# Kernel tuning notes

Measured on AMD Instinct MI355X. Metric: run time of the kernel, lower is better.

Reference implementation:

```python
import jax, jax.numpy as jnp
import numpy as np

H = 4096  # input_size == hidden_size


def setup_inputs() -> dict:
    key = jax.random.key(0)
    ks = jax.random.split(key, 11)
    s = 1.0 / np.sqrt(2 * H)  # nn.Linear default init scale
    return {
        "h_tmin1": jax.random.normal(ks[0], (H,), jnp.float32),
        "c_tmin1": jax.random.normal(ks[1], (H,), jnp.float32),
        "x_t": jax.random.normal(ks[2], (H,), jnp.float32),
        "W_f": jax.random.uniform(ks[3], (H, 2 * H), jnp.float32, -s, s),
        "b_f": jax.random.uniform(ks[4], (H,), jnp.float32, -s, s),
        "W_i": jax.random.uniform(ks[5], (H, 2 * H), jnp.float32, -s, s),
        "b_i": jax.random.uniform(ks[6], (H,), jnp.float32, -s, s),
        "W_C": jax.random.uniform(ks[7], (H, 2 * H), jnp.float32, -s, s),
        "b_C": jax.random.uniform(ks[8], (H,), jnp.float32, -s, s),
        "W_o": jax.random.uniform(ks[9], (H, 2 * H), jnp.float32, -s, s),
        "b_o": jax.random.uniform(ks[10], (H,), jnp.float32, -s, s),
    }


def reference(h_tmin1, c_tmin1, x_t, W_f, b_f, W_i, b_i, W_C, b_C, W_o, b_o):
    # z_hx = cat([h, x]) used for f, i, o gates.
    z_hx = jnp.concatenate([h_tmin1, x_t])          # [2H]
    # Faithful quirk: original C_t calls Ctilde_t(h_tmin1, c_tmin1),
    # so the candidate gate sees cat([h, c]) instead of cat([h, x]).
    z_hc = jnp.concatenate([h_tmin1, c_tmin1])      # [2H]

    f = jax.nn.sigmoid(W_f @ z_hx + b_f)            # forget gate  [H]
    i = jax.nn.sigmoid(W_i @ z_hx + b_i)            # input gate   [H]
    Ctilde = jnp.tanh(W_C @ z_hc + b_C)             # candidate    [H]
    C = f * c_tmin1 + i * Ctilde                    # new cell     [H]
    o = jax.nn.sigmoid(W_o @ z_hx + b_o)            # output gate  [H]
    h = o * jnp.tanh(C)                             # new hidden   [H]
    # output() returns (hidden, cell); it recomputes C_t redundantly in the
    # original, which is mathematically identical to reusing C here.
    return (h, C)
```

## Files before the change

kernel.cpp:

```cpp
#include <hip/hip_runtime.h>
#include <math.h>

constexpr int H  = 4096;
constexpr int H2 = 8192;

__global__ __launch_bounds__(256, 4)
void lstm_step_kernel(const float* __restrict__ h_prev,
                      const float* __restrict__ c_prev,
                      const float* __restrict__ x_t,
                      const float* __restrict__ W_f, const float* __restrict__ b_f,
                      const float* __restrict__ W_i, const float* __restrict__ b_i,
                      const float* __restrict__ W_C, const float* __restrict__ b_C,
                      const float* __restrict__ W_o, const float* __restrict__ b_o,
                      float* __restrict__ out)
{
    const int gtid = blockIdx.x * blockDim.x + threadIdx.x;
    const int row  = gtid >> 6;
    const int lane = threadIdx.x & 63;
    if (row >= H) return;

    const float4* wf = (const float4*)(W_f + (size_t)row * H2);
    const float4* wi = (const float4*)(W_i + (size_t)row * H2);
    const float4* wc = (const float4*)(W_C + (size_t)row * H2);
    const float4* wo = (const float4*)(W_o + (size_t)row * H2);
    const float4* hv = (const float4*)h_prev;
    const float4* xv = (const float4*)x_t;
    const float4* cv = (const float4*)c_prev;

    float4 af = make_float4(0.f, 0.f, 0.f, 0.f);
    float4 ai = make_float4(0.f, 0.f, 0.f, 0.f);
    float4 ac = make_float4(0.f, 0.f, 0.f, 0.f);
    float4 ao = make_float4(0.f, 0.f, 0.f, 0.f);

    #pragma unroll 4
    for (int it = 0; it < 16; ++it) {
        const int c = it * 64 + lane;
        const float4 z = hv[c];
        const float4 a = wf[c];
        const float4 b = wi[c];
        const float4 d = wc[c];
        const float4 e = wo[c];
        af.x = fmaf(a.x, z.x, af.x); af.y = fmaf(a.y, z.y, af.y);
        af.z = fmaf(a.z, z.z, af.z); af.w = fmaf(a.w, z.w, af.w);
        ai.x = fmaf(b.x, z.x, ai.x); ai.y = fmaf(b.y, z.y, ai.y);
        ai.z = fmaf(b.z, z.z, ai.z); ai.w = fmaf(b.w, z.w, ai.w);
        ac.x = fmaf(d.x, z.x, ac.x); ac.y = fmaf(d.y, z.y, ac.y);
        ac.z = fmaf(d.z, z.z, ac.z); ac.w = fmaf(d.w, z.w, ac.w);
        ao.x = fmaf(e.x, z.x, ao.x); ao.y = fmaf(e.y, z.y, ao.y);
        ao.z = fmaf(e.z, z.z, ao.z); ao.w = fmaf(e.w, z.w, ao.w);
    }

    #pragma unroll 4
    for (int it = 0; it < 16; ++it) {
        const int c  = it * 64 + lane;
        const int wc4 = 1024 + c;
        const float4 zx = xv[c];
        const float4 zc = cv[c];
        const float4 a = wf[wc4];
        const float4 b = wi[wc4];
        const float4 d = wc[wc4];
        const float4 e = wo[wc4];
        af.x = fmaf(a.x, zx.x, af.x); af.y = fmaf(a.y, zx.y, af.y);
        af.z = fmaf(a.z, zx.z, af.z); af.w = fmaf(a.w, zx.w, af.w);
        ai.x = fmaf(b.x, zx.x, ai.x); ai.y = fmaf(b.y, zx.y, ai.y);
        ai.z = fmaf(b.z, zx.z, ai.z); ai.w = fmaf(b.w, zx.w, ai.w);
        ac.x = fmaf(d.x, zc.x, ac.x); ac.y = fmaf(d.y, zc.y, ac.y);
        ac.z = fmaf(d.z, zc.z, ac.z); ac.w = fmaf(d.w, zc.w, ac.w);
        ao.x = fmaf(e.x, zx.x, ao.x); ao.y = fmaf(e.y, zx.y, ao.y);
        ao.z = fmaf(e.z, zx.z, ao.z); ao.w = fmaf(e.w, zx.w, ao.w);
    }

    float sf = (af.x + af.y) + (af.z + af.w);
    float si = (ai.x + ai.y) + (ai.z + ai.w);
    float sc = (ac.x + ac.y) + (ac.z + ac.w);
    float so = (ao.x + ao.y) + (ao.z + ao.w);

    #pragma unroll
    for (int off = 32; off > 0; off >>= 1) {
        sf += __shfl_down(sf, off, 64);
        si += __shfl_down(si, off, 64);
        sc += __shfl_down(sc, off, 64);
        so += __shfl_down(so, off, 64);
    }

    if (lane == 0) {
        const float f      = 1.f / (1.f + expf(-(sf + b_f[row])));
        const float ig     = 1.f / (1.f + expf(-(si + b_i[row])));
        const float ctilde = tanhf(sc + b_C[row]);
        const float og     = 1.f / (1.f + expf(-(so + b_o[row])));
        const float Cnew   = f * c_prev[row] + ig * ctilde;
        out[row]     = og * tanhf(Cnew);
        out[H + row] = Cnew;
    }
}

extern "C" void kernel_launch(void* const* d_in, const int* in_sizes, int n_in,
                              void* d_out, int out_size, void* d_ws, size_t ws_size,
                              hipStream_t stream) {
    const float* h_prev = (const float*)d_in[0];
    const float* c_prev = (const float*)d_in[1];
    const float* x_t    = (const float*)d_in[2];
    const float* W_f    = (const float*)d_in[3];
    const float* b_f    = (const float*)d_in[4];
    const float* W_i    = (const float*)d_in[5];
    const float* b_i    = (const float*)d_in[6];
    const float* W_C    = (const float*)d_in[7];
    const float* b_C    = (const float*)d_in[8];
    const float* W_o    = (const float*)d_in[9];
    const float* b_o    = (const float*)d_in[10];
    float* out = (float*)d_out;

    const int waves_needed = H;
    const int threads = 256;
    const int blocks  = (waves_needed * 64) / threads;
    lstm_step_kernel<<<blocks, threads, 0, stream>>>(
        h_prev, c_prev, x_t, W_f, b_f, W_i, b_i, W_C, b_C, W_o, b_o, out);
}
```

Before: 95.15 us.

## Split each gate row across two waves and combine partial sums in shared memory

Each output row's dot product is now split between two wavefronts: one handles the h half and one the x/c half. Their partial sums are combined through shared memory after a block barrier. This doubles the number of waves to give more memory parallelism for the bandwidth-bound GEMV. It also raises the launch-bounds occupancy hint and the unroll factor. In exchange it adds a __syncthreads, a shared-memory reduction and extra register pressure from the higher occupancy target.

Measured after the change: 117.3 us. +23.2%, slower.

```diff
diff --git a/kernel.cpp b/kernel.cpp
--- a/kernel.cpp
+++ b/kernel.cpp
@@ -4,7 +4,7 @@
 constexpr int H  = 4096;
 constexpr int H2 = 8192;
 
-__global__ __launch_bounds__(256, 4)
+__global__ __launch_bounds__(256, 8)
 void lstm_step_kernel(const float* __restrict__ h_prev,
                       const float* __restrict__ c_prev,
                       const float* __restrict__ x_t,
@@ -14,15 +14,19 @@
                       const float* __restrict__ W_o, const float* __restrict__ b_o,
                       float* __restrict__ out)
 {
-    const int gtid = blockIdx.x * blockDim.x + threadIdx.x;
-    const int row  = gtid >> 6;
+    __shared__ float part[4][4];
+
+    const int wid  = threadIdx.x >> 6;
     const int lane = threadIdx.x & 63;
-    if (row >= H) return;
+    const int row  = blockIdx.x * 2 + (wid >> 1);
+    const int half = wid & 1;
 
-    const float4* wf = (const float4*)(W_f + (size_t)row * H2);
-    const float4* wi = (const float4*)(W_i + (size_t)row * H2);
-    const float4* wc = (const float4*)(W_C + (size_t)row * H2);
-    const float4* wo = (const float4*)(W_o + (size_t)row * H2);
+    const size_t rowbase = (size_t)row * H2;
+    const int hoff = half * 1024;
+    const float4* wf = (const float4*)(W_f + rowbase) + hoff;
+    const float4* wi = (const float4*)(W_i + rowbase) + hoff;
+    const float4* wc = (const float4*)(W_C + rowbase) + hoff;
+    const float4* wo = (const float4*)(W_o + rowbase) + hoff;
     const float4* hv = (const float4*)h_prev;
     const float4* xv = (const float4*)x_t;
     const float4* cv = (const float4*)c_prev;
@@ -32,42 +36,43 @@
     float4 ac = make_float4(0.f, 0.f, 0.f, 0.f);
     float4 ao = make_float4(0.f, 0.f, 0.f, 0.f);
 
-    #pragma unroll 4
-    for (int it = 0; it < 16; ++it) {
-        const int c = it * 64 + lane;
-        const float4 z = hv[c];
-        const float4 a = wf[c];
-        const float4 b = wi[c];
-        const float4 d = wc[c];
-        const float4 e = wo[c];
-        af.x = fmaf(a.x, z.x, af.x); af.y = fmaf(a.y, z.y, af.y);
-        af.z = fmaf(a.z, z.z, af.z); af.w = fmaf(a.w, z.w, af.w);
-        ai.x = fmaf(b.x, z.x, ai.x); ai.y = fmaf(b.y, z.y, ai.y);
-        ai.z = fmaf(b.z, z.z, ai.z); ai.w = fmaf(b.w, z.w, ai.w);
-        ac.x = fmaf(d.x, z.x, ac.x); ac.y = fmaf(d.y, z.y, ac.y);
-        ac.z = fmaf(d.z, z.z, ac.z); ac.w = fmaf(d.w, z.w, ac.w);
-        ao.x = fmaf(e.x, z.x, ao.x); ao.y = fmaf(e.y, z.y, ao.y);
-        ao.z = fmaf(e.z, z.z, ao.z); ao.w = fmaf(e.w, z.w, ao.w);
-    }
-
-    #pragma unroll 4
-    for (int it = 0; it < 16; ++it) {
-        const int c  = it * 64 + lane;
-        const int wc4 = 1024 + c;
-        const float4 zx = xv[c];
-        const float4 zc = cv[c];
-        const float4 a = wf[wc4];
-        const float4 b = wi[wc4];
-        const float4 d = wc[wc4];
-        const float4 e = wo[wc4];
-        af.x = fmaf(a.x, zx.x, af.x); af.y = fmaf(a.y, zx.y, af.y);
-        af.z = fmaf(a.z, zx.z, af.z); af.w = fmaf(a.w, zx.w, af.w);
-        ai.x = fmaf(b.x, zx.x, ai.x); ai.y = fmaf(b.y, zx.y, ai.y);
-        ai.z = fmaf(b.z, zx.z, ai.z); ai.w = fmaf(b.w, zx.w, ai.w);
-        ac.x = fmaf(d.x, zc.x, ac.x); ac.y = fmaf(d.y, zc.y, ac.y);
-        ac.z = fmaf(d.z, zc.z, ac.z); ac.w = fmaf(d.w, zc.w, ac.w);
-        ao.x = fmaf(e.x, zx.x, ao.x); ao.y = fmaf(e.y, zx.y, ao.y);
-        ao.z = fmaf(e.z, zx.z, ao.z); ao.w = fmaf(e.w, zx.w, ao.w);
+    if (half == 0) {
+        #pragma unroll 8
+        for (int it = 0; it < 16; ++it) {
+            const int c = it * 64 + lane;
+            const float4 z = hv[c];
+            const float4 a = wf[c];
+            const float4 b = wi[c];
+            const float4 d = wc[c];
+            const float4 e = wo[c];
+            af.x = fmaf(a.x, z.x, af.x); af.y = fmaf(a.y, z.y, af.y);
+            af.z = fmaf(a.z, z.z, af.z); af.w = fmaf(a.w, z.w, af.w);
+            ai.x = fmaf(b.x, z.x, ai.x); ai.y = fmaf(b.y, z.y, ai.y);
+            ai.z = fmaf(b.z, z.z, ai.z); ai.w = fmaf(b.w, z.w, ai.w);
+            ac.x = fmaf(d.x, z.x, ac.x); ac.y = fmaf(d.y, z.y, ac.y);
+            ac.z = fmaf(d.z, z.z, ac.z); ac.w = fmaf(d.w, z.w, ac.w);
+            ao.x = fmaf(e.x, z.x, ao.x); ao.y = fmaf(e.y, z.y, ao.y);
+            ao.z = fmaf(e.z, z.z, ao.z); ao.w = fmaf(e.w, z.w, ao.w);
+        }
+    } else {
+        #pragma unroll 8
+        for (int it = 0; it < 16; ++it) {
+            const int c = it * 64 + lane;
+            const float4 zx = xv[c];
+            const float4 zc = cv[c];
+            const float4 a = wf[c];
+            const float4 b = wi[c];
+            const float4 d = wc[c];
+            const float4 e = wo[c];
+            af.x = fmaf(a.x, zx.x, af.x); af.y = fmaf(a.y, zx.y, af.y);
+            af.z = fmaf(a.z, zx.z, af.z); af.w = fmaf(a.w, zx.w, af.w);
+            ai.x = fmaf(b.x, zx.x, ai.x); ai.y = fmaf(b.y, zx.y, ai.y);
+            ai.z = fmaf(b.z, zx.z, ai.z); ai.w = fmaf(b.w, zx.w, ai.w);
+            ac.x = fmaf(d.x, zc.x, ac.x); ac.y = fmaf(d.y, zc.y, ac.y);
+            ac.z = fmaf(d.z, zc.z, ac.z); ac.w = fmaf(d.w, zc.w, ac.w);
+            ao.x = fmaf(e.x, zx.x, ao.x); ao.y = fmaf(e.y, zx.y, ao.y);
+            ao.z = fmaf(e.z, zx.z, ao.z); ao.w = fmaf(e.w, zx.w, ao.w);
+        }
     }
 
     float sf = (af.x + af.y) + (af.z + af.w);
@@ -84,13 +89,28 @@
     }
 
     if (lane == 0) {
-        const float f      = 1.f / (1.f + expf(-(sf + b_f[row])));
-        const float ig     = 1.f / (1.f + expf(-(si + b_i[row])));
-        const float ctilde = tanhf(sc + b_C[row]);
-        const float og     = 1.f / (1.f + expf(-(so + b_o[row])));
-        const float Cnew   = f * c_prev[row] + ig * ctilde;
-        out[row]     = og * tanhf(Cnew);
-        out[H + row] = Cnew;
+        part[wid][0] = sf;
+        part[wid][1] = si;
+        part[wid][2] = sc;
+        part[wid][3] = so;
+    }
+    __syncthreads();
+
+    if (threadIdx.x < 2) {
+        const int r  = blockIdx.x * 2 + (int)threadIdx.x;
+        const int w0 = (int)threadIdx.x * 2;
+        const float tf = part[w0][0] + part[w0 + 1][0];
+        const float ti = part[w0][1] + part[w0 + 1][1];
+        const float tc = part[w0][2] + part[w0 + 1][2];
+        const float to = part[w0][3] + part[w0 + 1][3];
+
+        const float f      = 1.f / (1.f + expf(-(tf + b_f[r])));
+        const float ig     = 1.f / (1.f + expf(-(ti + b_i[r])));
+        const float ctilde = tanhf(tc + b_C[r]);
+        const float og     = 1.f / (1.f + expf(-(to + b_o[r])));
+        const float Cnew   = f * c_prev[r] + ig * ctilde;
+        out[r]     = og * tanhf(Cnew);
+        out[H + r] = Cnew;
     }
 }
 
@@ -110,9 +130,6 @@
     const float* b_o    = (const float*)d_in[10];
     float* out = (float*)d_out;
 
-    const int waves_needed = H;
-    const int threads = 256;
-    const int blocks  = (waves_needed * 64) / threads;
-    lstm_step_kernel<<<blocks, threads, 0, stream>>>(
+    lstm_step_kernel<<<H / 2, 256, 0, stream>>>(
         h_prev, c_prev, x_t, W_f, b_f, W_i, b_i, W_C, b_C, W_o, b_o, out);
 }
```
